# Kernel tuning notes

Hardware: AMD Instinct MI355X
Metric: run time of the kernel (lower is better)

The kernel has to match this reference:

```python
import jax, jax.numpy as jnp
import numpy as np

H_DIM = 64
NUM_ROTATIONS = 128


def setup_inputs() -> dict:
    key = jax.random.key(0)
    k1, k2 = jax.random.split(key)
    x = jax.random.normal(k1, (8, 4096, 16, H_DIM), dtype=jnp.float32)
    thetas = jax.random.normal(k2, (NUM_ROTATIONS,), dtype=jnp.float32)
    return {"x": x, "thetas": thetas}


def reference(x, thetas):
    # x: [B, S, nH, h_dim]. Original does x @ G_k for k in range(num_rotations),
    # where G_k is identity except rows/cols (i, j) = (k % h, (k+1) % h):
    #   (xG)[:, i] =  cos*x_i + sin*x_j
    #   (xG)[:, j] = -sin*x_i + cos*x_j
    # Rotations are sequential (consecutive k share a column), so use lax.scan
    # and touch only the two affected columns instead of a full GEMM.
    B, S, nH, D = x.shape
    K = thetas.shape[0]
    xf = x.reshape(-1, D)  # [N, h_dim]
    ks = jnp.arange(K, dtype=jnp.int32)
    idx_i = ks % D
    idx_j = (ks + 1) % D

    def step(xc, inp):
        i, j, th = inp
        c, s = jnp.cos(th), jnp.sin(th)
        xi = xc[:, i]
        xj = xc[:, j]
        xc = xc.at[:, i].set(c * xi + s * xj).at[:, j].set(-s * xi + c * xj)
        return xc, None

    xf, _ = jax.lax.scan(step, xf, (idx_i, idx_j, thetas))
    return xf.reshape(B, S, nH, D)
```

## Files before the change

kernel.cpp:

```cpp
#include <hip/hip_runtime.h>

#define D_DIM 64
#define N_ROT 128

__global__ __launch_bounds__(64) void givens_kernel(
    const float* __restrict__ x,
    const float* __restrict__ thetas,
    float* __restrict__ out,
    int nchunks)
{
    __shared__ __align__(16) float buf[64 * D_DIM];
    __shared__ float2 cs_tab[N_ROT];

    const int l = threadIdx.x;
    const int lo16 = l & 15;

    {
        const float tha = thetas[l];
        const float thb = thetas[l + 64];
        cs_tab[l]      = make_float2(cosf(tha), sinf(tha));
        cs_tab[l + 64] = make_float2(cosf(thb), sinf(thb));
    }
    asm volatile("s_waitcnt lgkmcnt(0)" ::: "memory");

    for (int chunk = blockIdx.x; chunk < nchunks; chunk += gridDim.x) {
        const char* gin  = (const char*)(x   + (size_t)chunk * (64 * D_DIM));
        char*       gout = (char*)      (out + (size_t)chunk * (64 * D_DIM));

        #pragma unroll
        for (int q = 0; q < 16; ++q) {
            const int r = q * 4 + (l >> 4);
            const int g = lo16 ^ (r & 15);
            __builtin_amdgcn_global_load_lds(
                (const __attribute__((address_space(1))) void*)(gin + r * 256 + g * 16),
                (__attribute__((address_space(3))) void*)((char*)buf + q * 1024),
                16, 0, 0);
        }
        asm volatile("s_waitcnt vmcnt(0)" ::: "memory");

        float v[D_DIM];
        #pragma unroll
        for (int g = 0; g < 16; ++g) {
            const int sl = g ^ lo16;
            const float4 t = *reinterpret_cast<const float4*>(&buf[l * D_DIM + sl * 4]);
            v[4 * g + 0] = t.x; v[4 * g + 1] = t.y;
            v[4 * g + 2] = t.z; v[4 * g + 3] = t.w;
        }

        #pragma unroll
        for (int k = 0; k < N_ROT; ++k) {
            const int i = k & (D_DIM - 1);
            const int j = (k + 1) & (D_DIM - 1);
            const float2 cs = cs_tab[k];
            const float xi = v[i], xj = v[j];
            v[i] = fmaf(cs.x, xi,  cs.y * xj);
            v[j] = fmaf(cs.x, xj, -cs.y * xi);
        }

        #pragma unroll
        for (int g = 0; g < 16; ++g) {
            const int sl = g ^ lo16;
            float4 t;
            t.x = v[4 * g + 0]; t.y = v[4 * g + 1];
            t.z = v[4 * g + 2]; t.w = v[4 * g + 3];
            *reinterpret_cast<float4*>(&buf[l * D_DIM + sl * 4]) = t;
        }
        asm volatile("s_waitcnt lgkmcnt(0)" ::: "memory");

        #pragma unroll
        for (int q = 0; q < 16; ++q) {
            const int r = q * 4 + (l >> 4);
            const int g = lo16 ^ (r & 15);
            const float4 t = *reinterpret_cast<const float4*>(&buf[q * 256 + l * 4]);
            *reinterpret_cast<float4*>(gout + r * 256 + g * 16) = t;
        }
    }
}

extern "C" void kernel_launch(void* const* d_in, const int* in_sizes, int n_in,
                              void* d_out, int out_size, void* d_ws, size_t ws_size,
                              hipStream_t stream) {
    const float* x      = (const float*)d_in[0];
    const float* thetas = (const float*)d_in[1];
    float* out          = (float*)d_out;

    const int nrows   = in_sizes[0] / D_DIM;
    const int nchunks = nrows / 64;

    int grid = 9 * 256;
    if (grid > nchunks) grid = nchunks;

    givens_kernel<<<grid, 64, 0, stream>>>(x, thetas, out, nchunks);
}
```

Before: 54.36 us.

## Double-buffer LDS to prefetch next chunk during rotation compute

Splits the shared buffer into a load staging buffer and an output buffer. The next chunk's global-to-LDS load is issued before the current chunk's rotations, so memory latency overlaps with compute. Each block now processes a contiguous range of chunks instead of a grid stride, and the grid shrinks from 9*256 to 4*256 blocks. This doubles LDS per block and may lower occupancy, and the vmcnt(16) wait assumes a particular ordering of the outstanding counter, which must hold alongside the 16 global stores.

```diff
diff --git a/kernel.cpp b/kernel.cpp
--- a/kernel.cpp
+++ b/kernel.cpp
@@ -9,10 +9,11 @@
     float* __restrict__ out,
     int nchunks)
 {
-    __shared__ __align__(16) float buf[64 * D_DIM];
+    __shared__ __align__(16) float bufA[64 * D_DIM];
+    __shared__ __align__(16) float bufB[64 * D_DIM];
     __shared__ float2 cs_tab[N_ROT];
 
-    const int l = threadIdx.x;
+    const int l    = threadIdx.x;
     const int lo16 = l & 15;
 
     {
@@ -23,38 +24,51 @@
     }
     asm volatile("s_waitcnt lgkmcnt(0)" ::: "memory");
 
-    for (int chunk = blockIdx.x; chunk < nchunks; chunk += gridDim.x) {
-        const char* gin  = (const char*)(x   + (size_t)chunk * (64 * D_DIM));
-        char*       gout = (char*)      (out + (size_t)chunk * (64 * D_DIM));
+    const int cpb = (nchunks + gridDim.x - 1) / gridDim.x;
+    const int c0  = blockIdx.x * cpb;
+    const int c1  = (c0 + cpb < nchunks) ? (c0 + cpb) : nchunks;
+    if (c0 >= c1) return;
 
+    auto STAGE = [&](int c) {
+        const char* g = (const char*)(x + (size_t)c * (64 * D_DIM));
         #pragma unroll
         for (int q = 0; q < 16; ++q) {
-            const int r = q * 4 + (l >> 4);
-            const int g = lo16 ^ (r & 15);
+            const int r  = q * 4 + (l >> 4);
+            const int gs = lo16 ^ (r & 15);
             __builtin_amdgcn_global_load_lds(
-                (const __attribute__((address_space(1))) void*)(gin + r * 256 + g * 16),
-                (__attribute__((address_space(3))) void*)((char*)buf + q * 1024),
+                (const __attribute__((address_space(1))) void*)(g + r * 256 + gs * 16),
+                (__attribute__((address_space(3))) void*)((char*)bufA + q * 1024),
                 16, 0, 0);
         }
-        asm volatile("s_waitcnt vmcnt(0)" ::: "memory");
+    };
 
-        float v[D_DIM];
+    float v[D_DIM];
+
+    auto GATHER = [&]() {
         #pragma unroll
         for (int g = 0; g < 16; ++g) {
             const int sl = g ^ lo16;
-            const float4 t = *reinterpret_cast<const float4*>(&buf[l * D_DIM + sl * 4]);
+            const float4 t = *reinterpret_cast<const float4*>(&bufA[l * D_DIM + sl * 4]);
             v[4 * g + 0] = t.x; v[4 * g + 1] = t.y;
             v[4 * g + 2] = t.z; v[4 * g + 3] = t.w;
         }
+    };
 
+    STAGE(c0);
+    asm volatile("s_waitcnt vmcnt(0)" ::: "memory");
+    GATHER();
+    asm volatile("s_waitcnt lgkmcnt(0)" ::: "memory");
+    if (c0 + 1 < c1) STAGE(c0 + 1);
+
+    for (int c = c0; c < c1; ++c) {
         #pragma unroll
         for (int k = 0; k < N_ROT; ++k) {
             const int i = k & (D_DIM - 1);
             const int j = (k + 1) & (D_DIM - 1);
             const float2 cs = cs_tab[k];
             const float xi = v[i], xj = v[j];
-            v[i] = fmaf(cs.x, xi,  cs.y * xj);
-            v[j] = fmaf(cs.x, xj, -cs.y * xi);
+            v[i] = fmaf(cs.x, xi, cs.y * xj);
+            v[j] = fmaf(-cs.y, xi, cs.x * xj);
         }
 
         #pragma unroll
@@ -63,16 +77,26 @@
             float4 t;
             t.x = v[4 * g + 0]; t.y = v[4 * g + 1];
             t.z = v[4 * g + 2]; t.w = v[4 * g + 3];
-            *reinterpret_cast<float4*>(&buf[l * D_DIM + sl * 4]) = t;
+            *reinterpret_cast<float4*>(&bufB[l * D_DIM + sl * 4]) = t;
         }
         asm volatile("s_waitcnt lgkmcnt(0)" ::: "memory");
 
-        #pragma unroll
-        for (int q = 0; q < 16; ++q) {
-            const int r = q * 4 + (l >> 4);
-            const int g = lo16 ^ (r & 15);
-            const float4 t = *reinterpret_cast<const float4*>(&buf[q * 256 + l * 4]);
-            *reinterpret_cast<float4*>(gout + r * 256 + g * 16) = t;
+        {
+            char* gout = (char*)(out + (size_t)c * (64 * D_DIM));
+            #pragma unroll
+            for (int q = 0; q < 16; ++q) {
+                const int r  = q * 4 + (l >> 4);
+                const int gs = lo16 ^ (r & 15);
+                const float4 t = *reinterpret_cast<const float4*>(&bufB[q * 256 + l * 4]);
+                *reinterpret_cast<float4*>(gout + r * 256 + gs * 16) = t;
+            }
+        }
+
+        if (c + 1 < c1) {
+            asm volatile("s_waitcnt vmcnt(16)" ::: "memory");
+            GATHER();
+            asm volatile("s_waitcnt lgkmcnt(0)" ::: "memory");
+            if (c + 2 < c1) STAGE(c + 2);
         }
     }
 }
@@ -87,7 +111,7 @@
     const int nrows   = in_sizes[0] / D_DIM;
     const int nchunks = nrows / 64;
 
-    int grid = 9 * 256;
+    int grid = 4 * 256;
     if (grid > nchunks) grid = nchunks;
 
     givens_kernel<<<grid, 64, 0, stream>>>(x, thetas, out, nchunks);
```

New measurement: 49.76 us. 1.09x faster.
